# Kernel optimization log

Hardware: AMD Instinct MI355X
Metric: run time of the kernel (lower is better)

## Reference

```python
import jax, jax.numpy as jnp
import numpy as np

B, D, H, W, L = 32, 768, 14, 14, 77
TEMP_G, TEMP1, TEMP2, TEMP3 = 10.0, 4.0, 5.0, 10.0
LAMBDA_G, LAMBDA_L = 1.0, 1.0
EPS = 1e-8
NEG = -1e30


def setup_inputs() -> dict:
    key = jax.random.key(0)
    k1, k2, k3, k4, k5 = jax.random.split(key, 5)
    img_global = jax.random.normal(k1, (B, D), dtype=jnp.float32)
    img_local = jax.random.normal(k2, (B, D, H, W), dtype=jnp.float32)
    text_global = jax.random.normal(k3, (B, D), dtype=jnp.float32)
    text_local = jax.random.normal(k4, (B, L, D), dtype=jnp.float32)
    # ragged caption lengths: prefix attention mask, lengths in [10, L]
    lens = jax.random.randint(k5, (B,), 10, L + 1)
    attention_mask = (jnp.arange(L)[None, :] < lens[:, None]).astype(jnp.int32)
    return {"img_global": img_global, "img_local": img_local,
            "text_global": text_global, "text_local": text_local,
            "attention_mask": attention_mask}


def _ce_arange(scores):
    # cross entropy with labels = arange(n), mean reduction
    return jnp.mean(jax.nn.logsumexp(scores, axis=1) - jnp.diagonal(scores))


def _gloria_loss(img_global, img_local, text_global, text_local, attention_mask):
    mask = attention_mask.astype(bool)                      # [B, L]
    # ---- global contrastive loss ----
    in_ = img_global / jnp.maximum(jnp.linalg.norm(img_global, axis=1, keepdims=True), 1e-12)
    tn_ = text_global / jnp.maximum(jnp.linalg.norm(text_global, axis=1, keepdims=True), 1e-12)
    g_scores = (in_ @ tn_.T) * TEMP_G                       # [B, B]
    loss_global = 0.5 * (_ce_arange(g_scores) + _ce_arange(g_scores.T))

    # ---- local contrastive loss (vectorized over all text/image pairs) ----
    tl = jnp.swapaxes(text_local, 1, 2)                     # [B, D, L] (forward() transposes since L != D)
    ctx = img_local.reshape(B, D, H * W)                    # [B, D, S]
    # raw attention logits: text i words vs image j pixels -> [i, j, s, l]
    logits = jnp.einsum('jds,idl->ijsl', ctx, tl)
    logits = jnp.where(mask[:, None, None, :], logits, NEG)
    a1 = jax.nn.softmax(logits, axis=-1)                    # softmax over words (first softmax)
    a2 = jax.nn.softmax(TEMP1 * jnp.swapaxes(a1, 2, 3), axis=-1)  # [i, j, l, s], softmax over pixels
    wctx = jnp.einsum('jds,ijls->ijdl', ctx, a2)            # weighted context [i, j, D, l]
    # cosine similarity per word, over feature dim
    w12 = jnp.einsum('idl,ijdl->ijl', tl, wctx)
    n1 = jnp.linalg.norm(tl, axis=1)                        # [i, l]
    n2 = jnp.linalg.norm(wctx, axis=2)                      # [i, j, l]
    cos = w12 / jnp.maximum(n1[:, None, :] * n2, EPS)       # [i, j, l]
    row = jnp.exp(TEMP2 * cos) * mask[:, None, :]           # mask padded words
    sim = jnp.log(row.sum(axis=-1))                         # [i, j]  (local_agg='sum')
    # torch cats per-caption columns: similarities[j, i] -> transpose
    scores = sim.T * TEMP3                                  # [img j, text i]
    loss_local = 0.5 * (_ce_arange(scores) + _ce_arange(scores.T))

    return LAMBDA_G * loss_global + LAMBDA_L * loss_local


def reference(img_global, img_local, text_global, text_local, attention_mask):
    return _gloria_loss(img_global, img_local, text_global, text_local, attention_mask)
```

## Files before the change

### kernel.cpp

```cpp
#include <hip/hip_runtime.h>
#include <math.h>

#define NB 32
#define ND 768
#define NS 196
#define NL 77

typedef __bf16 bf16x8 __attribute__((ext_vector_type(8)));
typedef float f32x4 __attribute__((ext_vector_type(4)));

__device__ __forceinline__ f32x4 mfma16(bf16x8 a, bf16x8 b, f32x4 c) {
  return __builtin_amdgcn_mfma_f32_16x16x32_bf16(a, b, c, 0, 0, 0);
}

#define GLOAD16(gp, lp)                                          \
  __builtin_amdgcn_global_load_lds(                              \
      (const __attribute__((address_space(1))) void*)(gp),       \
      (__attribute__((address_space(3))) void*)(lp), 16, 0, 0)


__global__ __launch_bounds__(256) void prep_all_kernel(
    const float* __restrict__ text_local,
    const float* __restrict__ img_local,
    const int* __restrict__ amask,
    __bf16* __restrict__ txf, __bf16* __restrict__ cTf,
    float* __restrict__ n1ws, int* __restrict__ lenws) {
  const int bid = blockIdx.x;
  const int t = threadIdx.x;
  __shared__ float tile[64][213];

  if (bid < 960) {
    int tau = bid * 256 + t;
    int i = tau / 7680;
    int r = tau - i * 7680;
    int dk = r / 320;
    int r2 = r - dk * 320;
    int lt = r2 >> 6, lane = r2 & 63;
    int n16 = lane & 15, g = lane >> 4;
    int l = lt * 16 + n16;
    float v[8];
#pragma unroll
    for (int q = 0; q < 8; ++q) v[q] = 0.f;
    if (l < NL) {
      const float* src = text_local + ((size_t)i * NL + l) * ND + dk * 32 + g * 8;
      float4 a = *(const float4*)src;
      float4 b = *(const float4*)(src + 4);
      v[0] = a.x; v[1] = a.y; v[2] = a.z; v[3] = a.w;
      v[4] = b.x; v[5] = b.y; v[6] = b.z; v[7] = b.w;
    }
    bf16x8 hv, lv;
#pragma unroll
    for (int q = 0; q < 8; ++q) {
      __bf16 h = (__bf16)v[q];
      hv[q] = h;
      lv[q] = (__bf16)(v[q] - (float)h);
    }
    size_t base = ((((size_t)i * 24 + dk) * 5 + lt) * 2) * 512 + (size_t)lane * 8;
    *(bf16x8*)(txf + base) = hv;
    *(bf16x8*)(txf + base + 512) = lv;
  } else if (bid < 1344) {
    const int b2 = bid - 960;
    const int j = b2 / 12, dc = b2 - (b2 / 12) * 12;
    const float* src = img_local + ((size_t)j * ND + dc * 64) * NS;
    for (int idx = t; idx < 3136; idx += 256) {
      int dd = idx / 49, sq = idx - dd * 49;
      float4 v = *(const float4*)(src + (size_t)dd * NS + sq * 4);
      tile[dd][sq * 4 + 0] = v.x;
      tile[dd][sq * 4 + 1] = v.y;
      tile[dd][sq * 4 + 2] = v.z;
      tile[dd][sq * 4 + 3] = v.w;
    }
    __syncthreads();
    for (int idx = t; idx < 1664; idx += 256) {
      int lane = idx & 63;
      int rem = idx >> 6;
      int S = rem >> 1, dd2 = rem & 1;
      int n16 = lane & 15, g = lane >> 4;
      int s = S * 16 + n16;
      bf16x8 hv, lv;
#pragma unroll
      for (int e = 0; e < 8; ++e) {
        float v = (s < NS) ? tile[dd2 * 32 + g * 8 + e][s] : 0.f;
        __bf16 h = (__bf16)v;
        hv[e] = h;
        lv[e] = (__bf16)(v - (float)h);
      }
      int dk = dc * 2 + dd2;
      size_t base = ((((size_t)j * 13 + S) * 24 + dk) * 2) * 512 + (size_t)lane * 8;
      *(bf16x8*)(cTf + base) = hv;
      *(bf16x8*)(cTf + base + 512) = lv;
    }
  } else {
    const int i = bid - 1344;
    const int lane = t & 63, w = t >> 6;
    __shared__ int slen;
    if (t == 0) slen = 0;
    __syncthreads();
    if (t < NL && amask[i * NL + t] != 0) atomicAdd(&slen, 1);
    for (int l = w; l < NL; l += 4) {
      const float4* p = (const float4*)(text_local + ((size_t)i * NL + l) * ND);
      float s = 0.f;
#pragma unroll
      for (int k = 0; k < 3; ++k) {
        float4 v = p[lane + 64 * k];
        s += v.x * v.x + v.y * v.y + v.z * v.z + v.w * v.w;
      }
#pragma unroll
      for (int off = 32; off; off >>= 1) s += __shfl_xor(s, off);
      if (lane == 0) n1ws[i * 80 + l] = sqrtf(s);
    }
    __syncthreads();
    if (t == 0) lenws[i] = slen;
  }
}

__global__ void mid_kernel(const __bf16* __restrict__ cTf, __bf16* __restrict__ Gf,
                           const float* __restrict__ img_global,
                           const float* __restrict__ text_global,
                           float* __restrict__ gscw,
                           const int* __restrict__ lenws, int* __restrict__ ordws) {
  const int bid = blockIdx.x;
  const int t = threadIdx.x;
  __shared__ __align__(16) float shi[ND];

  if (bid < 832) {
    const int j = bid / 26;
    const int rr = bid - j * 26;
    const int st = rr >> 1, ch = rr & 1;
    const int lane = t & 63, w = t >> 6;
    const int g = lane >> 4, n16 = lane & 15;
    const f32x4 z4 = {0.f, 0.f, 0.f, 0.f};
    f32x4 accG[2];
    accG[0] = z4; accG[1] = z4;
    const int base = ch * 7;
    const int ncols = ch ? 6 : 7;
    const size_t cj = (size_t)j * 13;
    for (int dk = 0; dk < 24; ++dk) {
      size_t ao = ((cj + st) * 24 + dk) * 2 * 512 + (size_t)lane * 8;
      bf16x8 Ah = *(const bf16x8*)(cTf + ao);
      bf16x8 Al = *(const bf16x8*)(cTf + ao + 512);
#pragma unroll
      for (int q = 0; q < 2; ++q) {
        int ntl = w + (q << 2);
        if (ntl < ncols) {
          int nt = base + ntl;
          size_t bo = ((cj + nt) * 24 + dk) * 2 * 512 + (size_t)lane * 8;
          bf16x8 Bh = *(const bf16x8*)(cTf + bo);
          bf16x8 Bl = *(const bf16x8*)(cTf + bo + 512);
          accG[q] = mfma16(Ah, Bh, accG[q]);
          accG[q] = mfma16(Ah, Bl, accG[q]);
          accG[q] = mfma16(Al, Bh, accG[q]);
        }
      }
    }
#pragma unroll
    for (int q = 0; q < 2; ++q) {
      int ntl = w + (q << 2);
      int nt = base + ntl;
      bool compute = (ntl < ncols);
      bool zfill = (ch == 1 && nt == 13);
      if (compute || zfill) {
#pragma unroll
        for (int r = 0; r < 4; ++r) {
          int col = nt * 16 + n16;
          float v = compute ? accG[q][r] : 0.f;
          __bf16 hi = (__bf16)v;
          __bf16 lo = (__bf16)(v - (float)hi);
          int kt = col >> 5, gg = (col >> 3) & 3, e = col & 7;
          int lane2 = (g * 4 + r) + (gg << 4);
          size_t o = ((((size_t)j * 13 + st) * 7 + kt) * 2) * 512 + (size_t)lane2 * 8 + e;
          Gf[o] = hi;
          Gf[o + 512] = lo;
        }
      }
    }
  } else if (bid < 864) {
    const int a = bid - 832;
    const int lane = t & 63, w = t >> 6;
    if (t < ND / 4) ((float4*)shi)[t] = ((const float4*)(img_global + (size_t)a * ND))[t];
    __syncthreads();
    for (int b = w; b < NB; b += 4) {
      const float4* pt = (const float4*)(text_global + (size_t)b * ND);
      const float4* pi = (const float4*)shi;
      float dot = 0.f, ni = 0.f, nt = 0.f;
#pragma unroll
      for (int k = 0; k < 3; ++k) {
        float4 x = pi[lane + 64 * k];
        float4 y = pt[lane + 64 * k];
        dot += x.x * y.x + x.y * y.y + x.z * y.z + x.w * y.w;
        ni  += x.x * x.x + x.y * x.y + x.z * x.z + x.w * x.w;
        nt  += y.x * y.x + y.y * y.y + y.z * y.z + y.w * y.w;
      }
#pragma unroll
      for (int off = 32; off; off >>= 1) {
        dot += __shfl_xor(dot, off);
        ni  += __shfl_xor(ni, off);
        nt  += __shfl_xor(nt, off);
      }
      if (lane == 0)
        gscw[a * NB + b] = dot / fmaxf(sqrtf(ni), 1e-12f) / fmaxf(sqrtf(nt), 1e-12f) * 10.0f;
    }
  } else {
    if (t == 0) {
      int o[32];
      for (int k = 0; k < 32; ++k) o[k] = k;
      for (int x = 0; x < 31; ++x) {
        int best = x;
        for (int y = x + 1; y < 32; ++y)
          if (lenws[o[y]] > lenws[o[best]]) best = y;
        int tmp = o[x]; o[x] = o[best]; o[best] = tmp;
      }
      for (int k = 0; k < 32; ++k) ordws[k] = o[k];
    }
  }
}

__global__ __launch_bounds__(512, 4) void pair_kernel(
    const __bf16* __restrict__ txf, const __bf16* __restrict__ cTf,
    const __bf16* __restrict__ Gf,
    const float* __restrict__ n1ws, const int* __restrict__ lenws,
    const int* __restrict__ ordws,
    float* __restrict__ simws) {
  const int t = threadIdx.x;
  const int wg = ((blockIdx.x & 7) << 6) + (blockIdx.x >> 3);
  const int j = wg >> 4;
  const int m = wg & 15;
  const int i0 = ordws[m], i1 = ordws[31 - m];
  const int len0 = lenws[i0], len1 = lenws[i1];
  const int nlt0 = (len0 + 15) >> 4, nlt1 = (len1 + 15) >> 4;
  const int lane = t & 63, wid = t >> 6;
  const int g = lane >> 4, n16 = lane & 15;
  const bool vb = (wid < 5);

  __shared__ __align__(16) union {
    __bf16 e2f[7 * 5 * 64 * 8];
    __bf16 b1[2][2][5][2][512];
  } U;
  __shared__ float w12s[80], z2s[80], n2s[80];

  const f32x4 z4 = {0.f, 0.f, 0.f, 0.f};
  f32x4 acc[2][2][5];
#pragma unroll
  for (int p = 0; p < 2; ++p)
#pragma unroll
    for (int q = 0; q < 2; ++q)
#pragma unroll
      for (int lt = 0; lt < 5; ++lt) acc[p][q][lt] = z4;

  const __bf16* txi0 = txf + (size_t)i0 * 24 * 5 * 2 * 512;
  const __bf16* txi1 = txf + (size_t)i1 * 24 * 5 * 2 * 512;
  const size_t cj = (size_t)j * 13;

#pragma unroll
  for (int k = 0; k < 4; ++k) {
    int s = wid + ((k & 1) << 3);
    int c = (s < 10) ? s : (s - 10);
    int lt = c >> 1, pl = c & 1;
    const __bf16* tx = (k >> 1) ? txi1 : txi0;
    GLOAD16(tx + (((size_t)lt * 2 + pl) << 9) + ((size_t)lane << 3),
            &U.b1[0][k >> 1][lt][pl][0]);
  }
  __syncthreads();

#pragma unroll 1
  for (int dk = 0; dk < 24; ++dk) {
    const int cur = dk & 1;
    if (dk < 23) {
#pragma unroll
      for (int k = 0; k < 4; ++k) {
        int s = wid + ((k & 1) << 3);
        int c = (s < 10) ? s : (s - 10);
        int lt = c >> 1, pl = c & 1;
        const __bf16* tx = (k >> 1) ? txi1 : txi0;
        GLOAD16(tx + (((size_t)(dk + 1) * 5 + lt) * 2 + pl) * 512 + ((size_t)lane << 3),
                &U.b1[cur ^ 1][k >> 1][lt][pl][0]);
      }
    }
    {
      size_t ao = ((cj + wid) * 24 + dk) * 1024 + ((size_t)lane << 3);
      bf16x8 Ah = *(const bf16x8*)(cTf + ao);
      bf16x8 Al = *(const bf16x8*)(cTf + ao + 512);
      __builtin_amdgcn_s_setprio(1);
#pragma unroll
      for (int lt = 0; lt < 5; ++lt) {
        if (lt < nlt0) {
          bf16x8 Bh = *(const bf16x8*)&U.b1[cur][0][lt][0][lane << 3];
          bf16x8 Bl = *(const bf16x8*)&U.b1[cur][0][lt][1][lane << 3];
          acc[0][0][lt] = mfma16(Ah, Bh, acc[0][0][lt]);
          acc[0][0][lt] = mfma16(Ah, Bl, acc[0][0][lt]);
          acc[0][0][lt] = mfma16(Al, Bh, acc[0][0][lt]);
        }
        if (lt < nlt1) {
          bf16x8 Bh = *(const bf16x8*)&U.b1[cur][1][lt][0][lane << 3];
          bf16x8 Bl = *(const bf16x8*)&U.b1[cur][1][lt][1][lane << 3];
          acc[1][0][lt] = mfma16(Ah, Bh, acc[1][0][lt]);
          acc[1][0][lt] = mfma16(Ah, Bl, acc[1][0][lt]);
          acc[1][0][lt] = mfma16(Al, Bh, acc[1][0][lt]);
        }
      }
      __builtin_amdgcn_s_setprio(0);
    }
    if (vb) {
      size_t ao = ((cj + wid + 8) * 24 + dk) * 1024 + ((size_t)lane << 3);
      bf16x8 Ah = *(const bf16x8*)(cTf + ao);
      bf16x8 Al = *(const bf16x8*)(cTf + ao + 512);
      __builtin_amdgcn_s_setprio(1);
#pragma unroll
      for (int lt = 0; lt < 5; ++lt) {
        if (lt < nlt0) {
          bf16x8 Bh = *(const bf16x8*)&U.b1[cur][0][lt][0][lane << 3];
          bf16x8 Bl = *(const bf16x8*)&U.b1[cur][0][lt][1][lane << 3];
          acc[0][1][lt] = mfma16(Ah, Bh, acc[0][1][lt]);
          acc[0][1][lt] = mfma16(Ah, Bl, acc[0][1][lt]);
          acc[0][1][lt] = mfma16(Al, Bh, acc[0][1][lt]);
        }
        if (lt < nlt1) {
          bf16x8 Bh = *(const bf16x8*)&U.b1[cur][1][lt][0][lane << 3];
          bf16x8 Bl = *(const bf16x8*)&U.b1[cur][1][lt][1][lane << 3];
          acc[1][1][lt] = mfma16(Ah, Bh, acc[1][1][lt]);
          acc[1][1][lt] = mfma16(Ah, Bl, acc[1][1][lt]);
          acc[1][1][lt] = mfma16(Al, Bh, acc[1][1][lt]);
        }
      }
      __builtin_amdgcn_s_setprio(0);
    }
    __syncthreads();
  }

#pragma unroll
  for (int p = 0; p < 2; ++p) {
    const int ip   = p ? i1 : i0;
    const int lenp = p ? len1 : len0;
    const int nltp = p ? nlt1 : nlt0;

    __syncthreads();
    if (t < 80) { w12s[t] = 0.f; z2s[t] = 0.f; n2s[t] = 0.f; }
    for (int idx = t; idx < 2240; idx += 512)
      ((uint4*)U.e2f)[idx] = make_uint4(0, 0, 0, 0);
    __syncthreads();

    float w12loc[5], z2loc[5];
#pragma unroll
    for (int lt = 0; lt < 5; ++lt) { w12loc[lt] = 0.f; z2loc[lt] = 0.f; }
#pragma unroll
    for (int q = 0; q < 2; ++q) {
      const int S = wid + (q << 3);
      if (q == 0 || vb) {
#pragma unroll
        for (int r = 0; r < 4; ++r) {
          int s = S * 16 + g * 4 + r;
          bool srow = (s < NS);
          float mx = -1e30f;
#pragma unroll
          for (int lt = 0; lt < 5; ++lt) {
            if (lt < nltp) {
              if ((lt * 16 + n16) < lenp) mx = fmaxf(mx, acc[p][q][lt][r]);
            }
          }
          mx = fmaxf(mx, __shfl_xor(mx, 1));
          mx = fmaxf(mx, __shfl_xor(mx, 2));
          mx = fmaxf(mx, __shfl_xor(mx, 4));
          mx = fmaxf(mx, __shfl_xor(mx, 8));
          float z = 0.f;
          float ev[5];
#pragma unroll
          for (int lt = 0; lt < 5; ++lt) {
            float e = 0.f;
            if (lt < nltp) {
              if ((lt * 16 + n16) < lenp) e = __expf(acc[p][q][lt][r] - mx);
            }
            ev[lt] = e;
            z += e;
          }
          z += __shfl_xor(z, 1);
          z += __shfl_xor(z, 2);
          z += __shfl_xor(z, 4);
          z += __shfl_xor(z, 8);
          float inv = 4.0f / z;
#pragma unroll
          for (int lt = 0; lt < 5; ++lt) {
            if (lt < nltp) {
              if (((lt * 16 + n16) < lenp) && srow) {
                float e2 = __expf(ev[lt] * inv);
                w12loc[lt] += e2 * acc[p][q][lt][r];
                z2loc[lt] += e2;
                int kt = s >> 5, kk = s & 31;
                U.e2f[(((kt * 5) + lt) * 64 + (n16 + ((kk >> 3) << 4))) * 8 + (kk & 7)] = (__bf16)e2;
              }
            }
          }
        }
      }
    }
#pragma unroll
    for (int lt = 0; lt < 5; ++lt) {
      w12loc[lt] += __shfl_xor(w12loc[lt], 16);
      w12loc[lt] += __shfl_xor(w12loc[lt], 32);
      z2loc[lt] += __shfl_xor(z2loc[lt], 16);
      z2loc[lt] += __shfl_xor(z2loc[lt], 32);
    }
    if (lane < 16) {
#pragma unroll
      for (int lt = 0; lt < 5; ++lt) {
        if (lt < nltp) {
          atomicAdd(&w12s[lt * 16 + lane], w12loc[lt]);
          atomicAdd(&z2s[lt * 16 + lane], z2loc[lt]);
        }
      }
    }
    __syncthreads();

    float n2loc[5];
#pragma unroll
    for (int lt = 0; lt < 5; ++lt) n2loc[lt] = 0.f;
#pragma unroll
    for (int q = 0; q < 2; ++q) {
      const int S = wid + (q << 3);
      if (q == 0 || vb) {
        f32x4 a2[5];
#pragma unroll
        for (int lt = 0; lt < 5; ++lt) a2[lt] = z4;
        const __bf16* gp = Gf + (((size_t)j * 13 + S) * 7) * 1024 + ((size_t)lane << 3);
        bf16x8 GAh = *(const bf16x8*)gp;
        bf16x8 GAl = *(const bf16x8*)(gp + 512);
#pragma unroll
        for (int kt = 0; kt < 7; ++kt) {
          bf16x8 GAhN, GAlN;
          if (kt < 6) {
            GAhN = *(const bf16x8*)(gp + (size_t)(kt + 1) * 1024);
            GAlN = *(const bf16x8*)(gp + (size_t)(kt + 1) * 1024 + 512);
          }
          __builtin_amdgcn_s_setprio(1);
#pragma unroll
          for (int lt = 0; lt < 5; ++lt) {
            if (lt < nltp) {
              bf16x8 Bv = *(const bf16x8*)&U.e2f[(((kt * 5) + lt) * 64 + lane) * 8];
              a2[lt] = mfma16(GAh, Bv, a2[lt]);
              a2[lt] = mfma16(GAl, Bv, a2[lt]);
            }
          }
          __builtin_amdgcn_s_setprio(0);
          if (kt < 6) { GAh = GAhN; GAl = GAlN; }
        }
#pragma unroll
        for (int lt = 0; lt < 5; ++lt) {
          if (lt < nltp) {
#pragma unroll
            for (int r = 0; r < 4; ++r) {
              int s = S * 16 + g * 4 + r;
              int kt = s >> 5, kk = s & 31;
              float e2v = (float)U.e2f[(((kt * 5) + lt) * 64 + (n16 + ((kk >> 3) << 4))) * 8 + (kk & 7)];
              n2loc[lt] += e2v * a2[lt][r];
            }
          }
        }
      }
    }
#pragma unroll
    for (int lt = 0; lt < 5; ++lt) {
      n2loc[lt] += __shfl_xor(n2loc[lt], 16);
      n2loc[lt] += __shfl_xor(n2loc[lt], 32);
    }
    if (lane < 16) {
#pragma unroll
      for (int lt = 0; lt < 5; ++lt) {
        if (lt < nltp) atomicAdd(&n2s[lt * 16 + lane], n2loc[lt]);
      }
    }
    __syncthreads();

    if (t < lenp) {
      float z2 = z2s[t];
      float w12v = w12s[t] / z2;
      float n2v = sqrtf(n2s[t]) / z2;
      float n1v = n1ws[ip * 80 + t];
      float cosv = w12v / fmaxf(n1v * n2v, 1e-8f);
      w12s[t] = __expf(5.0f * cosv);
    }
    __syncthreads();
    if (wid == 0) {
      float e = (lane < lenp) ? w12s[lane] : 0.f;
      if (lane + 64 < lenp) e += w12s[lane + 64];
      e += __shfl_xor(e, 1);
      e += __shfl_xor(e, 2);
      e += __shfl_xor(e, 4);
      e += __shfl_xor(e, 8);
      e += __shfl_xor(e, 16);
      e += __shfl_xor(e, 32);
      if (lane == 0) simws[ip * NB + j] = __logf(e);
    }
  }
}

__global__ void loss_kernel(const float* __restrict__ gscw,
                            const float* __restrict__ simws,
                            float* __restrict__ out) {
  const int t = threadIdx.x;
  __shared__ float gs[NB][NB];
  __shared__ float sl[NB][NB];
  __shared__ float parts[4][NB];
  {
    float4 gv = ((const float4*)gscw)[t];
    ((float4*)gs)[t] = gv;
    float4 v = ((const float4*)simws)[t];
    int ii = t >> 3;
    int j0 = (t & 7) * 4;
    sl[j0 + 0][ii] = v.x * 10.0f;
    sl[j0 + 1][ii] = v.y * 10.0f;
    sl[j0 + 2][ii] = v.z * 10.0f;
    sl[j0 + 3][ii] = v.w * 10.0f;
  }
  __syncthreads();
  if (t < NB) {
    float m, z;
    m = -1e30f;
    for (int c = 0; c < NB; ++c) m = fmaxf(m, gs[t][c]);
    z = 0.f;
    for (int c = 0; c < NB; ++c) z += __expf(gs[t][c] - m);
    parts[0][t] = m + __logf(z) - gs[t][t];

    m = -1e30f;
    for (int c = 0; c < NB; ++c) m = fmaxf(m, gs[c][t]);
    z = 0.f;
    for (int c = 0; c < NB; ++c) z += __expf(gs[c][t] - m);
    parts[1][t] = m + __logf(z) - gs[t][t];

    m = -1e30f;
    for (int c = 0; c < NB; ++c) m = fmaxf(m, sl[t][c]);
    z = 0.f;
    for (int c = 0; c < NB; ++c) z += __expf(sl[t][c] - m);
    parts[2][t] = m + __logf(z) - sl[t][t];

    m = -1e30f;
    for (int c = 0; c < NB; ++c) m = fmaxf(m, sl[c][t]);
    z = 0.f;
    for (int c = 0; c < NB; ++c) z += __expf(sl[c][t] - m);
    parts[3][t] = m + __logf(z) - sl[t][t];
  }
  __syncthreads();
  if (t == 0) {
    float s0 = 0.f, s1 = 0.f, s2 = 0.f, s3 = 0.f;
    for (int r = 0; r < NB; ++r) {
      s0 += parts[0][r]; s1 += parts[1][r];
      s2 += parts[2][r]; s3 += parts[3][r];
    }
    out[0] = 0.5f * (s0 + s1) / 32.0f + 0.5f * (s2 + s3) / 32.0f;
  }
}

extern "C" void kernel_launch(void* const* d_in, const int* in_sizes, int n_in,
                              void* d_out, int out_size, void* d_ws, size_t ws_size,
                              hipStream_t stream) {
  (void)in_sizes; (void)n_in; (void)out_size; (void)ws_size;
  const float* img_global  = (const float*)d_in[0];
  const float* img_local   = (const float*)d_in[1];
  const float* text_global = (const float*)d_in[2];
  const float* text_local  = (const float*)d_in[3];
  const int*   amask       = (const int*)d_in[4];

  __bf16* txf = (__bf16*)d_ws;
  __bf16* cTf = txf + (size_t)3932160;
  __bf16* Gf  = cTf + (size_t)10223616;
  float* fsm  = (float*)(Gf + (size_t)2981888);
  float* n1ws  = fsm;
  float* simws = fsm + 2560;
  float* gscw  = fsm + 3584;
  int*   lenws = (int*)(fsm + 4608);
  int*   ordws = (int*)(fsm + 4640);

  prep_all_kernel<<<1376, 256, 0, stream>>>(text_local, img_local, amask,
                                            txf, cTf, n1ws, lenws);
  mid_kernel<<<865, 256, 0, stream>>>(cTf, Gf, img_global, text_global,
                                      gscw, lenws, ordws);
  pair_kernel<<<512, 512, 0, stream>>>(txf, cTf, Gf, n1ws, lenws, ordws, simws);
  loss_kernel<<<1, 256, 0, stream>>>(gscw, simws, (float*)d_out);
}
```

Measured before the change: 147.2 us.

## Merge pair-kernel MFMA loops, hoist A loads, halve prep LDS tile

The pair kernel now issues the global loads for both image A fragments at the top of each dk step, ahead of the async text prefetch. It then runs a single MFMA loop in which each B fragment read from LDS feeds both A fragments, so the shared-memory B reads per step are halved. The launch bound drops from 4 to 3 blocks per SM so the extra live registers fit. In the prep kernel, the image transpose tile is processed in two 32-row halves, halving its LDS footprint at the cost of an extra sync pair. Lower occupancy may reduce latency hiding in the pair kernel.

Measured after the change: 138.9 us. 5.6% less time.

```diff
diff --git a/kernel.cpp b/kernel.cpp
--- a/kernel.cpp
+++ b/kernel.cpp
@@ -27,7 +27,7 @@
     float* __restrict__ n1ws, int* __restrict__ lenws) {
   const int bid = blockIdx.x;
   const int t = threadIdx.x;
-  __shared__ float tile[64][213];
+  __shared__ float tile[32][213];
 
   if (bid < 960) {
     int tau = bid * 256 + t;
@@ -62,33 +62,36 @@
     const int b2 = bid - 960;
     const int j = b2 / 12, dc = b2 - (b2 / 12) * 12;
     const float* src = img_local + ((size_t)j * ND + dc * 64) * NS;
-    for (int idx = t; idx < 3136; idx += 256) {
-      int dd = idx / 49, sq = idx - dd * 49;
-      float4 v = *(const float4*)(src + (size_t)dd * NS + sq * 4);
-      tile[dd][sq * 4 + 0] = v.x;
-      tile[dd][sq * 4 + 1] = v.y;
-      tile[dd][sq * 4 + 2] = v.z;
-      tile[dd][sq * 4 + 3] = v.w;
-    }
-    __syncthreads();
-    for (int idx = t; idx < 1664; idx += 256) {
-      int lane = idx & 63;
-      int rem = idx >> 6;
-      int S = rem >> 1, dd2 = rem & 1;
-      int n16 = lane & 15, g = lane >> 4;
-      int s = S * 16 + n16;
-      bf16x8 hv, lv;
-#pragma unroll
-      for (int e = 0; e < 8; ++e) {
-        float v = (s < NS) ? tile[dd2 * 32 + g * 8 + e][s] : 0.f;
-        __bf16 h = (__bf16)v;
-        hv[e] = h;
-        lv[e] = (__bf16)(v - (float)h);
-      }
-      int dk = dc * 2 + dd2;
-      size_t base = ((((size_t)j * 13 + S) * 24 + dk) * 2) * 512 + (size_t)lane * 8;
-      *(bf16x8*)(cTf + base) = hv;
-      *(bf16x8*)(cTf + base + 512) = lv;
+#pragma unroll 1
+    for (int h = 0; h < 2; ++h) {
+      __syncthreads();
+      for (int idx = t; idx < 1568; idx += 256) {
+        int dd = idx / 49, sq = idx - dd * 49;
+        float4 v = *(const float4*)(src + (size_t)(h * 32 + dd) * NS + sq * 4);
+        tile[dd][sq * 4 + 0] = v.x;
+        tile[dd][sq * 4 + 1] = v.y;
+        tile[dd][sq * 4 + 2] = v.z;
+        tile[dd][sq * 4 + 3] = v.w;
+      }
+      __syncthreads();
+      const int dk = dc * 2 + h;
+      for (int idx = t; idx < 832; idx += 256) {
+        int lane = idx & 63;
+        int S = idx >> 6;
+        int n16 = lane & 15, g = lane >> 4;
+        int s = S * 16 + n16;
+        bf16x8 hv, lv;
+#pragma unroll
+        for (int e = 0; e < 8; ++e) {
+          float v = (s < NS) ? tile[g * 8 + e][s] : 0.f;
+          __bf16 hh = (__bf16)v;
+          hv[e] = hh;
+          lv[e] = (__bf16)(v - (float)hh);
+        }
+        size_t base = ((((size_t)j * 13 + S) * 24 + dk) * 2) * 512 + (size_t)lane * 8;
+        *(bf16x8*)(cTf + base) = hv;
+        *(bf16x8*)(cTf + base + 512) = lv;
+      }
     }
   } else {
     const int i = bid - 1344;
@@ -215,7 +218,7 @@
   }
 }
 
-__global__ __launch_bounds__(512, 4) void pair_kernel(
+__global__ __launch_bounds__(512, 3) void pair_kernel(
     const __bf16* __restrict__ txf, const __bf16* __restrict__ cTf,
     const __bf16* __restrict__ Gf,
     const float* __restrict__ n1ws, const int* __restrict__ lenws,
@@ -265,6 +268,17 @@
 #pragma unroll 1
   for (int dk = 0; dk < 24; ++dk) {
     const int cur = dk & 1;
+    bf16x8 Aha, Ala, Ahb, Alb;
+    {
+      size_t ao = ((cj + wid) * 24 + dk) * 1024 + ((size_t)lane << 3);
+      Aha = *(const bf16x8*)(cTf + ao);
+      Ala = *(const bf16x8*)(cTf + ao + 512);
+    }
+    if (vb) {
+      size_t ao = ((cj + wid + 8) * 24 + dk) * 1024 + ((size_t)lane << 3);
+      Ahb = *(const bf16x8*)(cTf + ao);
+      Alb = *(const bf16x8*)(cTf + ao + 512);
+    }
     if (dk < 23) {
 #pragma unroll
       for (int k = 0; k < 4; ++k) {
@@ -276,54 +290,35 @@
                 &U.b1[cur ^ 1][k >> 1][lt][pl][0]);
       }
     }
-    {
-      size_t ao = ((cj + wid) * 24 + dk) * 1024 + ((size_t)lane << 3);
-      bf16x8 Ah = *(const bf16x8*)(cTf + ao);
-      bf16x8 Al = *(const bf16x8*)(cTf + ao + 512);
-      __builtin_amdgcn_s_setprio(1);
-#pragma unroll
-      for (int lt = 0; lt < 5; ++lt) {
-        if (lt < nlt0) {
-          bf16x8 Bh = *(const bf16x8*)&U.b1[cur][0][lt][0][lane << 3];
-          bf16x8 Bl = *(const bf16x8*)&U.b1[cur][0][lt][1][lane << 3];
-          acc[0][0][lt] = mfma16(Ah, Bh, acc[0][0][lt]);
-          acc[0][0][lt] = mfma16(Ah, Bl, acc[0][0][lt]);
-          acc[0][0][lt] = mfma16(Al, Bh, acc[0][0][lt]);
-        }
-        if (lt < nlt1) {
-          bf16x8 Bh = *(const bf16x8*)&U.b1[cur][1][lt][0][lane << 3];
-          bf16x8 Bl = *(const bf16x8*)&U.b1[cur][1][lt][1][lane << 3];
-          acc[1][0][lt] = mfma16(Ah, Bh, acc[1][0][lt]);
-          acc[1][0][lt] = mfma16(Ah, Bl, acc[1][0][lt]);
-          acc[1][0][lt] = mfma16(Al, Bh, acc[1][0][lt]);
-        }
-      }
-      __builtin_amdgcn_s_setprio(0);
-    }
-    if (vb) {
-      size_t ao = ((cj + wid + 8) * 24 + dk) * 1024 + ((size_t)lane << 3);
-      bf16x8 Ah = *(const bf16x8*)(cTf + ao);
-      bf16x8 Al = *(const bf16x8*)(cTf + ao + 512);
-      __builtin_amdgcn_s_setprio(1);
-#pragma unroll
-      for (int lt = 0; lt < 5; ++lt) {
-        if (lt < nlt0) {
-          bf16x8 Bh = *(const bf16x8*)&U.b1[cur][0][lt][0][lane << 3];
-          bf16x8 Bl = *(const bf16x8*)&U.b1[cur][0][lt][1][lane << 3];
-          acc[0][1][lt] = mfma16(Ah, Bh, acc[0][1][lt]);
-          acc[0][1][lt] = mfma16(Ah, Bl, acc[0][1][lt]);
-          acc[0][1][lt] = mfma16(Al, Bh, acc[0][1][lt]);
-        }
-        if (lt < nlt1) {
-          bf16x8 Bh = *(const bf16x8*)&U.b1[cur][1][lt][0][lane << 3];
-          bf16x8 Bl = *(const bf16x8*)&U.b1[cur][1][lt][1][lane << 3];
-          acc[1][1][lt] = mfma16(Ah, Bh, acc[1][1][lt]);
-          acc[1][1][lt] = mfma16(Ah, Bl, acc[1][1][lt]);
-          acc[1][1][lt] = mfma16(Al, Bh, acc[1][1][lt]);
-        }
-      }
-      __builtin_amdgcn_s_setprio(0);
-    }
+    __builtin_amdgcn_s_setprio(1);
+#pragma unroll
+    for (int lt = 0; lt < 5; ++lt) {
+      if (lt < nlt0) {
+        bf16x8 Bh = *(const bf16x8*)&U.b1[cur][0][lt][0][lane << 3];
+        bf16x8 Bl = *(const bf16x8*)&U.b1[cur][0][lt][1][lane << 3];
+        acc[0][0][lt] = mfma16(Aha, Bh, acc[0][0][lt]);
+        acc[0][0][lt] = mfma16(Aha, Bl, acc[0][0][lt]);
+        acc[0][0][lt] = mfma16(Ala, Bh, acc[0][0][lt]);
+        if (vb) {
+          acc[0][1][lt] = mfma16(Ahb, Bh, acc[0][1][lt]);
+          acc[0][1][lt] = mfma16(Ahb, Bl, acc[0][1][lt]);
+          acc[0][1][lt] = mfma16(Alb, Bh, acc[0][1][lt]);
+        }
+      }
+      if (lt < nlt1) {
+        bf16x8 Bh = *(const bf16x8*)&U.b1[cur][1][lt][0][lane << 3];
+        bf16x8 Bl = *(const bf16x8*)&U.b1[cur][1][lt][1][lane << 3];
+        acc[1][0][lt] = mfma16(Aha, Bh, acc[1][0][lt]);
+        acc[1][0][lt] = mfma16(Aha, Bl, acc[1][0][lt]);
+        acc[1][0][lt] = mfma16(Ala, Bh, acc[1][0][lt]);
+        if (vb) {
+          acc[1][1][lt] = mfma16(Ahb, Bh, acc[1][1][lt]);
+          acc[1][1][lt] = mfma16(Ahb, Bl, acc[1][1][lt]);
+          acc[1][1][lt] = mfma16(Alb, Bh, acc[1][1][lt]);
+        }
+      }
+    }
+    __builtin_amdgcn_s_setprio(0);
     __syncthreads();
   }
 
```
